# Kernel optimization log

Measured on AMD Instinct MI355X. Metric: run time of the kernel, lower is better.

Reference implementation:

```python
import jax, jax.numpy as jnp
import numpy as np
import math

B, S, H = 2, 2048, 1024
NH, HD = 16, 64
EPS = 1e-12


def setup_inputs() -> dict:
    key = jax.random.key(0)
    ks = jax.random.split(key, 6)
    scale = 1.0 / math.sqrt(H)
    return {
        "hidden_states": jax.random.normal(ks[0], (B, S, H), jnp.float32),
        "Wq": jax.random.normal(ks[1], (H, H), jnp.float32) * scale,
        "bq": jnp.zeros((H,), jnp.float32),
        "Wk": jax.random.normal(ks[2], (H, H), jnp.float32) * scale,
        "bk": jnp.zeros((H,), jnp.float32),
        "Wv": jax.random.normal(ks[3], (H, H), jnp.float32) * scale,
        "bv": jnp.zeros((H,), jnp.float32),
        "Wo": jax.random.normal(ks[4], (H, H), jnp.float32) * scale,
        "bo": jnp.zeros((H,), jnp.float32),
        "gamma": jnp.ones((H,), jnp.float32),
        "beta": jnp.zeros((H,), jnp.float32),
    }


def _heads(x):
    # [B, S, H] -> [B, NH, S, HD]
    return x.reshape(B, S, NH, HD).transpose(0, 2, 1, 3)


def reference(hidden_states, Wq, bq, Wk, bk, Wv, bv, Wo, bo, gamma, beta):
    q = _heads(hidden_states @ Wq + bq)
    k = _heads(hidden_states @ Wk + bk)
    v = _heads(hidden_states @ Wv + bv)
    # scores: [B, NH, S, S]
    scores = jnp.einsum("bhqd,bhkd->bhqk", q, k) / math.sqrt(HD)
    probs = jax.nn.softmax(scores, axis=-1)
    ctx = jnp.einsum("bhqk,bhkd->bhqd", probs, v)
    ctx = ctx.transpose(0, 2, 1, 3).reshape(B, S, H)
    attn_out = ctx @ Wo + bo
    x = attn_out + hidden_states
    mu = jnp.mean(x, axis=-1, keepdims=True)
    var = jnp.var(x, axis=-1, keepdims=True)
    return (x - mu) / jnp.sqrt(var + EPS) * gamma + beta
```

## Files before the change

kernel.cpp:

```cpp
#include <hip/hip_runtime.h>
#include <hip/hip_bf16.h>

#define B_ 2
#define S_ 2048
#define H_ 1024
#define NH_ 16
#define HD_ 64
#define M_ (B_*S_)

typedef __attribute__((ext_vector_type(8))) short bf16x8;
typedef __attribute__((ext_vector_type(4))) short bf16x4;
typedef __attribute__((ext_vector_type(4))) float f32x4;
typedef __attribute__((ext_vector_type(4))) int   i32x4;

__device__ inline float waveReduceSum(float v) {
#pragma unroll
  for (int off = 32; off >= 1; off >>= 1) v += __shfl_xor(v, off);
  return v;
}

__device__ inline short f2bf(float f) {
  union { float f; unsigned u; } v; v.f = f;
  unsigned r = v.u + 0x7fffu + ((v.u >> 16) & 1u);
  return (short)(r >> 16);
}

__device__ inline unsigned cvt_pk_bf16(float lo, float hi) {
  unsigned w;
  asm("v_cvt_pk_bf16_f32 %0, %1, %2" : "=v"(w) : "v"(lo), "v"(hi));
  return w;
}

__device__ inline void async_load16(const void* g, void* l) {
  __builtin_amdgcn_global_load_lds(
      (const __attribute__((address_space(1))) void*)g,
      (__attribute__((address_space(3))) void*)l, 16, 0, 0);
}

__device__ inline int swz8(int r) { return (r & 3) | (((r >> 3) & 1) << 2); }

__global__ __launch_bounds__(256)
void cvt_bf16(const float* __restrict__ in, short* __restrict__ out) {
  const size_t i = (size_t)blockIdx.x * 256 + threadIdx.x;
  float4 v = ((const float4*)in)[i];
  bf16x4 o;
  o[0] = f2bf(v.x); o[1] = f2bf(v.y); o[2] = f2bf(v.z); o[3] = f2bf(v.w);
  ((bf16x4*)out)[i] = o;
}

__global__ __launch_bounds__(256)
void transpose_w4(const float* __restrict__ W0, const float* __restrict__ W1,
                  const float* __restrict__ W2, const float* __restrict__ W3,
                  short* __restrict__ Tqkv, short* __restrict__ To) {
  const float* W; short* T;
  switch (blockIdx.z) {
    case 0: W = W0; T = Tqkv; break;
    case 1: W = W1; T = Tqkv + (size_t)1024 * 1024; break;
    case 2: W = W2; T = Tqkv + (size_t)2048 * 1024; break;
    default: W = W3; T = To; break;
  }
  __shared__ float tile[32][36];
  const int tid = threadIdx.x;
  const int tx = tid & 7, ty = tid >> 3;
  const int k0 = blockIdx.y << 5, n0 = blockIdx.x << 5;
  float4 v = *(const float4*)&W[(size_t)(k0 + ty) * H_ + n0 + (tx << 2)];
  tile[ty][(tx << 2) + 0] = v.x;
  tile[ty][(tx << 2) + 1] = v.y;
  tile[ty][(tx << 2) + 2] = v.z;
  tile[ty][(tx << 2) + 3] = v.w;
  __syncthreads();
  bf16x4 o;
  o[0] = f2bf(tile[(tx << 2) + 0][ty]);
  o[1] = f2bf(tile[(tx << 2) + 1][ty]);
  o[2] = f2bf(tile[(tx << 2) + 2][ty]);
  o[3] = f2bf(tile[(tx << 2) + 3][ty]);
  *(bf16x4*)&T[(size_t)(n0 + ty) * H_ + k0 + (tx << 2)] = o;
}

__global__ __launch_bounds__(256)
void gemm_qkv(const short* __restrict__ A, const short* __restrict__ Bt,
              const float* __restrict__ bq, const float* __restrict__ bk,
              const float* __restrict__ bv, short* __restrict__ Qo,
              short* __restrict__ Ko, short* __restrict__ Vto) {
  __shared__ short A_lds[2][128][32];
  __shared__ short B_lds[2][128][32];
  const int tid = threadIdx.x;
  const int lane = tid & 63, wv = tid >> 6;
  const int l16 = lane & 15, lg = lane >> 4;
  const int wr = wv >> 1, wc = wv & 1;
  const int swzb = (blockIdx.x & 7) * 96 + (blockIdx.x >> 3);
  const int bx = swzb % 24, by = swzb / 24;
  const int m0 = by << 7, n0 = bx << 7;
  const int K = H_;

  const int srow = lane >> 2, soff = (lane & 3) << 3;

  f32x4 acc[4][4] = {};

#pragma unroll
  for (int i = 0; i < 2; ++i) {
    const int c = 2 * wv + i;
    async_load16(A + (size_t)(m0 + 16 * c + srow) * K + soff, &A_lds[0][16 * c][0]);
    async_load16(Bt + (size_t)(n0 + 16 * c + srow) * K + soff, &B_lds[0][16 * c][0]);
  }

  int cur = 0;
  for (int t = 0; t < K / 32; ++t) {
    __syncthreads();
    if (t + 1 < K / 32) {
      const int k0 = (t + 1) << 5;
#pragma unroll
      for (int i = 0; i < 2; ++i) {
        const int c = 2 * wv + i;
        async_load16(A + (size_t)(m0 + 16 * c + srow) * K + k0 + soff,
                     &A_lds[cur ^ 1][16 * c][0]);
        async_load16(Bt + (size_t)(n0 + 16 * c + srow) * K + k0 + soff,
                     &B_lds[cur ^ 1][16 * c][0]);
      }
    }
    bf16x8 af[4], bfr[4];
#pragma unroll
    for (int i = 0; i < 4; ++i)
      af[i] = *(const bf16x8*)&A_lds[cur][64 * wr + 16 * i + l16][8 * lg];
#pragma unroll
    for (int j = 0; j < 4; ++j)
      bfr[j] = *(const bf16x8*)&B_lds[cur][64 * wc + 16 * j + l16][8 * lg];
#pragma unroll
    for (int i = 0; i < 4; ++i)
#pragma unroll
      for (int j = 0; j < 4; ++j)
        acc[i][j] = __builtin_amdgcn_mfma_f32_16x16x32_bf16(af[i], bfr[j], acc[i][j], 0, 0, 0);
    cur ^= 1;
  }

  const int mt = n0 >> 10;
  const float* bias = (mt == 0) ? bq : (mt == 1 ? bk : bv);
  const float qs = (mt == 0) ? 0.125f * 1.4426950408889634f : 1.0f;

  if (mt < 2) {
    short* Out = (mt == 0) ? Qo : Ko;
#pragma unroll
    for (int i = 0; i < 4; ++i) {
#pragma unroll
      for (int j = 0; j < 4; ++j) {
        const int nl = (n0 & 1023) + 64 * wc + 16 * j + l16;
        const float bvl = bias[nl];
        const int h = nl >> 6, d = nl & 63;
#pragma unroll
        for (int r = 0; r < 4; ++r) {
          const int m = m0 + 64 * wr + 16 * i + 4 * lg + r;
          const int b = m >> 11, s = m & (S_ - 1);
          Out[(((size_t)(b * NH_ + h) * S_ + s) << 6) + d] =
              f2bf((acc[i][j][r] + bvl) * qs);
        }
      }
    }
  } else {
#pragma unroll
    for (int i = 0; i < 4; ++i) {
      const int mb = m0 + 64 * wr + 16 * i + 4 * lg;
      const int b = mb >> 11, s = mb & (S_ - 1);
#pragma unroll
      for (int j = 0; j < 4; ++j) {
        const int nl = (n0 & 1023) + 64 * wc + 16 * j + l16;
        const float bvl = bias[nl];
        const int h = nl >> 6, d = nl & 63;
        bf16x4 pk;
#pragma unroll
        for (int r = 0; r < 4; ++r) pk[r] = f2bf(acc[i][j][r] + bvl);
        *(bf16x4*)&Vto[(((size_t)(b * NH_ + h) * HD_ + d) << 11) + s] = pk;
      }
    }
  }
}

__global__ __launch_bounds__(256)
void gemm_o(const short* __restrict__ A, const short* __restrict__ Bt,
            const float* __restrict__ bias, float* __restrict__ C) {
  __shared__ short A_lds[2][64][32];
  __shared__ short B_lds[2][128][32];
  const int tid = threadIdx.x;
  const int lane = tid & 63, wv = tid >> 6;
  const int l16 = lane & 15, lg = lane >> 4;
  const int wr = wv >> 1, wc = wv & 1;
  const int swzb = (blockIdx.x & 7) * 64 + (blockIdx.x >> 3);
  const int bx = swzb & 7, by = swzb >> 3;
  const int m0 = by << 6, n0 = bx << 7;
  const int K = H_;

  const int srow = lane >> 2, soff = (lane & 3) << 3;

  f32x4 acc[2][4] = {};

  async_load16(A + (size_t)(m0 + 16 * wv + srow) * K + soff, &A_lds[0][16 * wv][0]);
#pragma unroll
  for (int i = 0; i < 2; ++i) {
    const int c = 2 * wv + i;
    async_load16(Bt + (size_t)(n0 + 16 * c + srow) * K + soff, &B_lds[0][16 * c][0]);
  }

  int cur = 0;
  for (int t = 0; t < K / 32; ++t) {
    __syncthreads();
    if (t + 1 < K / 32) {
      const int k0 = (t + 1) << 5;
      async_load16(A + (size_t)(m0 + 16 * wv + srow) * K + k0 + soff,
                   &A_lds[cur ^ 1][16 * wv][0]);
#pragma unroll
      for (int i = 0; i < 2; ++i) {
        const int c = 2 * wv + i;
        async_load16(Bt + (size_t)(n0 + 16 * c + srow) * K + k0 + soff,
                     &B_lds[cur ^ 1][16 * c][0]);
      }
    }
    bf16x8 af[2], bfr[4];
#pragma unroll
    for (int i = 0; i < 2; ++i)
      af[i] = *(const bf16x8*)&A_lds[cur][32 * wr + 16 * i + l16][8 * lg];
#pragma unroll
    for (int j = 0; j < 4; ++j)
      bfr[j] = *(const bf16x8*)&B_lds[cur][64 * wc + 16 * j + l16][8 * lg];
#pragma unroll
    for (int i = 0; i < 2; ++i)
#pragma unroll
      for (int j = 0; j < 4; ++j)
        acc[i][j] = __builtin_amdgcn_mfma_f32_16x16x32_bf16(af[i], bfr[j], acc[i][j], 0, 0, 0);
    cur ^= 1;
  }

#pragma unroll
  for (int i = 0; i < 2; ++i)
#pragma unroll
    for (int j = 0; j < 4; ++j) {
      const int n = n0 + 64 * wc + 16 * j + l16;
      const float bvl = bias[n];
#pragma unroll
      for (int r = 0; r < 4; ++r) {
        const int m = m0 + 32 * wr + 16 * i + 4 * lg + r;
        C[(size_t)m * H_ + n] = acc[i][j][r] + bvl;
      }
    }
}

__global__ __launch_bounds__(256)
void attn_mfma(const short* __restrict__ Qg, const short* __restrict__ Kg,
               const short* __restrict__ Vtg, short* __restrict__ ctxb) {
  __shared__ short K_lds[2][2][64][64];
  __shared__ short V_t[2][2][64][64];

  const int tid  = threadIdx.x;
  const int lane = tid & 63;
  const int wv   = tid >> 6;
  const int l16  = lane & 15, lg = lane >> 4;

  const int swz = (blockIdx.x & 7) * 128 + (blockIdx.x >> 3);
  const int bh = swz >> 5, qb = swz & 31;

  const short* Qh = Qg + ((size_t)bh * S_ << 6);
  const short* Kh = Kg + ((size_t)bh * S_ << 6);
  const short* Vh = Vtg + ((size_t)bh << 6) * S_;

  const int q0 = qb * 64 + wv * 16;

  bf16x8 qf[2];
  qf[0] = *(const bf16x8*)&Qh[((size_t)(q0 + l16) << 6) + 8 * lg];
  qf[1] = *(const bf16x8*)&Qh[((size_t)(q0 + l16) << 6) + 8 * lg + 32];

  const int l16part = ((l16 >> 2) << 3) + (l16 & 3);

  const int kr = tid >> 2;
  const int cb = (tid & 3) << 1;
  const int sz = swz8(kr);
  const int c1 = ((cb    ) ^ sz) << 3;
  const int c2 = ((cb + 1) ^ sz) << 3;

  f32x4 o[4] = {};
  float m_run = -1e30f, l_run = 0.f;

#pragma unroll
  for (int h = 0; h < 2; ++h) {
    const size_t kg = ((size_t)(64 * h + kr)) << 6;
    *(bf16x8*)&K_lds[0][h][kr][c1] = *(const bf16x8*)&Kh[kg + (cb << 3)];
    *(bf16x8*)&K_lds[0][h][kr][c2] = *(const bf16x8*)&Kh[kg + ((cb + 1) << 3)];
    const size_t vg = (size_t)kr * S_ + 64 * h;
    *(bf16x8*)&V_t[0][h][kr][c1]   = *(const bf16x8*)&Vh[vg + (cb << 3)];
    *(bf16x8*)&V_t[0][h][kr][c2]   = *(const bf16x8*)&Vh[vg + ((cb + 1) << 3)];
  }

  int cur = 0;
  for (int t = 0; t < S_ / 128; ++t) {
    bf16x8 nk[2][2], nv[2][2];
    const bool pre = (t + 1 < S_ / 128);
    if (pre) {
      const int kvn = (t + 1) * 128;
#pragma unroll
      for (int h = 0; h < 2; ++h) {
        const size_t kb = ((size_t)(kvn + 64 * h + kr)) << 6;
        nk[h][0] = *(const bf16x8*)&Kh[kb + (cb << 3)];
        nk[h][1] = *(const bf16x8*)&Kh[kb + ((cb + 1) << 3)];
        const size_t vb = (size_t)kr * S_ + kvn + 64 * h;
        nv[h][0] = *(const bf16x8*)&Vh[vb + (cb << 3)];
        nv[h][1] = *(const bf16x8*)&Vh[vb + ((cb + 1) << 3)];
      }
    }
    __syncthreads();

    f32x4 s[2][4] = {};
    __builtin_amdgcn_s_setprio(1);
#pragma unroll
    for (int h = 0; h < 2; ++h)
#pragma unroll
      for (int ks = 0; ks < 2; ++ks)
#pragma unroll
        for (int tt = 0; tt < 4; ++tt) {
          const int krow = ((tt >> 1) << 5) + ((tt & 1) << 2) + l16part;
          const int kch = (lg + 4 * ks) ^ swz8(krow);
          bf16x8 kf = *(const bf16x8*)&K_lds[cur][h][krow][kch << 3];
          s[h][tt] = __builtin_amdgcn_mfma_f32_16x16x32_bf16(kf, qf[ks], s[h][tt], 0, 0, 0);
        }
    __builtin_amdgcn_s_setprio(0);

    float pmax = -1e30f;
#pragma unroll
    for (int h = 0; h < 2; ++h)
#pragma unroll
      for (int tt = 0; tt < 4; ++tt)
        pmax = fmaxf(pmax, fmaxf(fmaxf(s[h][tt][0], s[h][tt][1]),
                                 fmaxf(s[h][tt][2], s[h][tt][3])));
    pmax = fmaxf(pmax, __shfl_xor(pmax, 16));
    pmax = fmaxf(pmax, __shfl_xor(pmax, 32));

    float p[2][4][4];
    float rs = 0.f;
    if (__any(pmax - m_run > 8.0f)) {
      const float mn = fmaxf(m_run, pmax);
      const float scl = __builtin_amdgcn_exp2f(m_run - mn);
      m_run = mn;
#pragma unroll
      for (int h = 0; h < 2; ++h)
#pragma unroll
        for (int tt = 0; tt < 4; ++tt)
#pragma unroll
          for (int r = 0; r < 4; ++r) {
            p[h][tt][r] = __builtin_amdgcn_exp2f(s[h][tt][r] - mn);
            rs += p[h][tt][r];
          }
      rs += __shfl_xor(rs, 16);
      rs += __shfl_xor(rs, 32);
      l_run = l_run * scl + rs;
      float sclr[4];
#pragma unroll
      for (int r = 0; r < 4; ++r) sclr[r] = __shfl(scl, 4 * lg + r);
#pragma unroll
      for (int tt = 0; tt < 4; ++tt)
#pragma unroll
        for (int r = 0; r < 4; ++r) o[tt][r] *= sclr[r];
    } else {
#pragma unroll
      for (int h = 0; h < 2; ++h)
#pragma unroll
        for (int tt = 0; tt < 4; ++tt)
#pragma unroll
          for (int r = 0; r < 4; ++r) {
            p[h][tt][r] = __builtin_amdgcn_exp2f(s[h][tt][r] - m_run);
            rs += p[h][tt][r];
          }
      rs += __shfl_xor(rs, 16);
      rs += __shfl_xor(rs, 32);
      l_run += rs;
    }

    unsigned w[2][4][2];
#pragma unroll
    for (int h = 0; h < 2; ++h)
#pragma unroll
      for (int tt = 0; tt < 4; ++tt) {
        w[h][tt][0] = cvt_pk_bf16(p[h][tt][0], p[h][tt][1]);
        w[h][tt][1] = cvt_pk_bf16(p[h][tt][2], p[h][tt][3]);
      }

    __builtin_amdgcn_s_setprio(1);
#pragma unroll
    for (int h = 0; h < 2; ++h)
#pragma unroll
      for (int ks = 0; ks < 2; ++ks) {
        i32x4 aw;
        aw[0] = (int)w[h][2 * ks][0];
        aw[1] = (int)w[h][2 * ks][1];
        aw[2] = (int)w[h][2 * ks + 1][0];
        aw[3] = (int)w[h][2 * ks + 1][1];
        const bf16x8 pf = __builtin_bit_cast(bf16x8, aw);
#pragma unroll
        for (int tt = 0; tt < 4; ++tt) {
          const int vrow = 16 * tt + l16;
          const int vch = (lg + 4 * ks) ^ swz8(vrow);
          bf16x8 vf = *(const bf16x8*)&V_t[cur][h][vrow][vch << 3];
          o[tt] = __builtin_amdgcn_mfma_f32_16x16x32_bf16(pf, vf, o[tt], 0, 0, 0);
        }
      }
    __builtin_amdgcn_s_setprio(0);

    if (pre) {
#pragma unroll
      for (int h = 0; h < 2; ++h) {
        *(bf16x8*)&K_lds[cur ^ 1][h][kr][c1] = nk[h][0];
        *(bf16x8*)&K_lds[cur ^ 1][h][kr][c2] = nk[h][1];
        *(bf16x8*)&V_t[cur ^ 1][h][kr][c1]   = nv[h][0];
        *(bf16x8*)&V_t[cur ^ 1][h][kr][c2]   = nv[h][1];
      }
    }
    cur ^= 1;
  }

  float invr[4];
#pragma unroll
  for (int r = 0; r < 4; ++r) invr[r] = 1.f / __shfl(l_run, 4 * lg + r);
  const int b = bh >> 4, h = bh & 15;
#pragma unroll
  for (int r = 0; r < 4; ++r) {
    const int q = q0 + 4 * lg + r;
#pragma unroll
    for (int tt = 0; tt < 4; ++tt)
      ctxb[(((size_t)(b * S_ + q) * NH_ + h) << 6) + 16 * tt + l16] =
          f2bf(o[tt][r] * invr[r]);
  }
}

__global__ __launch_bounds__(256)
void resid_ln(const float* __restrict__ attn_out, const float* __restrict__ hs,
              const float* __restrict__ gamma, const float* __restrict__ beta,
              float* __restrict__ out) {
  __shared__ float reds[4], reds2[4];
  const int row = blockIdx.x;
  const int tid = threadIdx.x;
  const float4* a4 = (const float4*)(attn_out + ((size_t)row << 10));
  const float4* h4 = (const float4*)(hs + ((size_t)row << 10));
  float4 a = a4[tid], h = h4[tid];
  float e0 = a.x + h.x, e1 = a.y + h.y, e2 = a.z + h.z, e3 = a.w + h.w;
  float s  = e0 + e1 + e2 + e3;
  float sq = e0 * e0 + e1 * e1 + e2 * e2 + e3 * e3;
  s = waveReduceSum(s);
  sq = waveReduceSum(sq);
  const int lane = tid & 63, wave = tid >> 6;
  if (lane == 0) { reds[wave] = s; reds2[wave] = sq; }
  __syncthreads();
  const float S1 = reds[0] + reds[1] + reds[2] + reds[3];
  const float S2 = reds2[0] + reds2[1] + reds2[2] + reds2[3];
  const float mu = S1 * (1.f / H_);
  const float var = S2 * (1.f / H_) - mu * mu;
  const float rstd = rsqrtf(var + 1e-12f);
  const float4 g = ((const float4*)gamma)[tid];
  const float4 bb = ((const float4*)beta)[tid];
  float4 o;
  o.x = (e0 - mu) * rstd * g.x + bb.x;
  o.y = (e1 - mu) * rstd * g.y + bb.y;
  o.z = (e2 - mu) * rstd * g.z + bb.z;
  o.w = (e3 - mu) * rstd * g.w + bb.w;
  ((float4*)(out + ((size_t)row << 10)))[tid] = o;
}

extern "C" void kernel_launch(void* const* d_in, const int* in_sizes, int n_in,
                              void* d_out, int out_size, void* d_ws, size_t ws_size,
                              hipStream_t stream) {
  const float* X     = (const float*)d_in[0];
  const float* Wq    = (const float*)d_in[1];
  const float* bq    = (const float*)d_in[2];
  const float* Wk    = (const float*)d_in[3];
  const float* bk    = (const float*)d_in[4];
  const float* Wv    = (const float*)d_in[5];
  const float* bv    = (const float*)d_in[6];
  const float* Wo    = (const float*)d_in[7];
  const float* bo    = (const float*)d_in[8];
  const float* gamma = (const float*)d_in[9];
  const float* beta  = (const float*)d_in[10];
  float* out = (float*)d_out;

  char* ws = (char*)d_ws;
  short* Xbf  = (short*)ws;
  short* Wqkv = (short*)(ws + ( 8u << 20));
  short* Wto  = (short*)(ws + (14u << 20));
  short* Qbf  = (short*)(ws + (16u << 20));
  short* Kbf  = (short*)(ws + (24u << 20));
  short* Vt   = (short*)(ws + (32u << 20));
  short* ctxb = Xbf;
  float* attn = (float*)(ws + (16u << 20));

  dim3 blk(256);
  hipLaunchKernelGGL(cvt_bf16, dim3((M_ * H_) / 1024), blk, 0, stream, X, Xbf);
  hipLaunchKernelGGL(transpose_w4, dim3(32, 32, 4), blk, 0, stream,
                     Wq, Wk, Wv, Wo, Wqkv, Wto);
  hipLaunchKernelGGL(gemm_qkv, dim3(768), blk, 0, stream,
                     Xbf, Wqkv, bq, bk, bv, Qbf, Kbf, Vt);
  hipLaunchKernelGGL(attn_mfma, dim3(1024), blk, 0, stream, Qbf, Kbf, Vt, ctxb);
  hipLaunchKernelGGL(gemm_o, dim3(512), blk, 0, stream, ctxb, Wto, bo, attn);
  hipLaunchKernelGGL(resid_ln, dim3(M_), blk, 0, stream, attn, X, gamma, beta, out);
}
```

Baseline: 244.4 us.

## Enlarge QKV GEMM tile to 256x256 with 512 threads and explicit pipelining

The QKV projection GEMM moves from 128x128 tiles with 256 threads to 256x256 tiles with 512 threads (8 waves, 128x64 each), cutting the grid from 768 to 192 blocks. The load loop becomes a two-stage prefetch with explicit vmcnt waits, raw s_barrier calls, sched_barrier fences and setprio around the MFMA block. The goal is more operand reuse per LDS load and better overlap of global loads with MFMA work. In exchange, 192 blocks may leave part of the 256 CUs idle, and the 8x4 accumulator per wave raises register pressure.

```diff
diff --git a/kernel.cpp b/kernel.cpp
--- a/kernel.cpp
+++ b/kernel.cpp
@@ -77,61 +77,77 @@
   *(bf16x4*)&T[(size_t)(n0 + ty) * H_ + k0 + (tx << 2)] = o;
 }
 
-__global__ __launch_bounds__(256)
+#define QKV_NT 32
+
+__global__ __launch_bounds__(512)
 void gemm_qkv(const short* __restrict__ A, const short* __restrict__ Bt,
               const float* __restrict__ bq, const float* __restrict__ bk,
               const float* __restrict__ bv, short* __restrict__ Qo,
               short* __restrict__ Ko, short* __restrict__ Vto) {
-  __shared__ short A_lds[2][128][32];
-  __shared__ short B_lds[2][128][32];
+  __shared__ short A_lds[2][256][32];
+  __shared__ short B_lds[2][256][32];
   const int tid = threadIdx.x;
   const int lane = tid & 63, wv = tid >> 6;
   const int l16 = lane & 15, lg = lane >> 4;
-  const int wr = wv >> 1, wc = wv & 1;
-  const int swzb = (blockIdx.x & 7) * 96 + (blockIdx.x >> 3);
-  const int bx = swzb % 24, by = swzb / 24;
-  const int m0 = by << 7, n0 = bx << 7;
+  const int wr = wv >> 2, wc = wv & 3;
+  const int swzb = (blockIdx.x & 7) * 24 + (blockIdx.x >> 3);
+  const int bx = swzb % 12, by = swzb / 12;
+  const int m0 = by << 8, n0 = bx << 8;
   const int K = H_;
 
-  const int srow = lane >> 2, soff = (lane & 3) << 3;
-
-  f32x4 acc[4][4] = {};
-
-#pragma unroll
-  for (int i = 0; i < 2; ++i) {
-    const int c = 2 * wv + i;
-    async_load16(A + (size_t)(m0 + 16 * c + srow) * K + soff, &A_lds[0][16 * c][0]);
-    async_load16(Bt + (size_t)(n0 + 16 * c + srow) * K + soff, &B_lds[0][16 * c][0]);
-  }
-
-  int cur = 0;
-  for (int t = 0; t < K / 32; ++t) {
-    __syncthreads();
-    if (t + 1 < K / 32) {
-      const int k0 = (t + 1) << 5;
-#pragma unroll
-      for (int i = 0; i < 2; ++i) {
-        const int c = 2 * wv + i;
-        async_load16(A + (size_t)(m0 + 16 * c + srow) * K + k0 + soff,
-                     &A_lds[cur ^ 1][16 * c][0]);
-        async_load16(Bt + (size_t)(n0 + 16 * c + srow) * K + k0 + soff,
-                     &B_lds[cur ^ 1][16 * c][0]);
-      }
-    }
-    bf16x8 af[4], bfr[4];
-#pragma unroll
-    for (int i = 0; i < 4; ++i)
-      af[i] = *(const bf16x8*)&A_lds[cur][64 * wr + 16 * i + l16][8 * lg];
+  const int srow = lane >> 2;
+  const int sch  = lane & 3;
+
+#define QKV_STAGE(buf, t_)                                                     \
+  {                                                                            \
+    const int k0_ = (t_) << 5;                                                 \
+    _Pragma("unroll")                                                          \
+    for (int i_ = 0; i_ < 2; ++i_) {                                           \
+      const int r0_ = 128 * i_ + 16 * wv;                                      \
+      async_load16(A + (size_t)(m0 + r0_ + srow) * K + k0_ + (sch << 3),       \
+                   &A_lds[buf][r0_][0]);                                       \
+      async_load16(Bt + (size_t)(n0 + r0_ + srow) * K + k0_ + (sch << 3),      \
+                   &B_lds[buf][r0_][0]);                                       \
+    }                                                                          \
+  }
+
+  f32x4 acc[8][4] = {};
+
+  QKV_STAGE(0, 0)
+  QKV_STAGE(1, 1)
+  asm volatile("s_waitcnt vmcnt(4)" ::: "memory");
+  __builtin_amdgcn_s_barrier();
+  __builtin_amdgcn_sched_barrier(0);
+
+  for (int t = 0; t < QKV_NT; ++t) {
+    const int cur = t & 1;
+    bf16x8 af[8], bfr[4];
+#pragma unroll
+    for (int i = 0; i < 8; ++i)
+      af[i] = *(const bf16x8*)&A_lds[cur][128 * wr + 16 * i + l16][8 * lg];
 #pragma unroll
     for (int j = 0; j < 4; ++j)
       bfr[j] = *(const bf16x8*)&B_lds[cur][64 * wc + 16 * j + l16][8 * lg];
-#pragma unroll
-    for (int i = 0; i < 4; ++i)
+    __builtin_amdgcn_s_setprio(1);
+#pragma unroll
+    for (int i = 0; i < 8; ++i)
 #pragma unroll
       for (int j = 0; j < 4; ++j)
         acc[i][j] = __builtin_amdgcn_mfma_f32_16x16x32_bf16(af[i], bfr[j], acc[i][j], 0, 0, 0);
-    cur ^= 1;
-  }
+    __builtin_amdgcn_s_setprio(0);
+    __builtin_amdgcn_sched_barrier(0);
+    __builtin_amdgcn_s_barrier();
+    __builtin_amdgcn_sched_barrier(0);
+    if (t + 2 < QKV_NT) {
+      QKV_STAGE(cur, t + 2)
+      asm volatile("s_waitcnt vmcnt(4)" ::: "memory");
+    } else {
+      asm volatile("s_waitcnt vmcnt(0)" ::: "memory");
+    }
+    __builtin_amdgcn_s_barrier();
+    __builtin_amdgcn_sched_barrier(0);
+  }
+#undef QKV_STAGE
 
   const int mt = n0 >> 10;
   const float* bias = (mt == 0) ? bq : (mt == 1 ? bk : bv);
@@ -140,7 +156,7 @@
   if (mt < 2) {
     short* Out = (mt == 0) ? Qo : Ko;
 #pragma unroll
-    for (int i = 0; i < 4; ++i) {
+    for (int i = 0; i < 8; ++i) {
 #pragma unroll
       for (int j = 0; j < 4; ++j) {
         const int nl = (n0 & 1023) + 64 * wc + 16 * j + l16;
@@ -148,7 +164,7 @@
         const int h = nl >> 6, d = nl & 63;
 #pragma unroll
         for (int r = 0; r < 4; ++r) {
-          const int m = m0 + 64 * wr + 16 * i + 4 * lg + r;
+          const int m = m0 + 128 * wr + 16 * i + 4 * lg + r;
           const int b = m >> 11, s = m & (S_ - 1);
           Out[(((size_t)(b * NH_ + h) * S_ + s) << 6) + d] =
               f2bf((acc[i][j][r] + bvl) * qs);
@@ -157,8 +173,8 @@
     }
   } else {
 #pragma unroll
-    for (int i = 0; i < 4; ++i) {
-      const int mb = m0 + 64 * wr + 16 * i + 4 * lg;
+    for (int i = 0; i < 8; ++i) {
+      const int mb = m0 + 128 * wr + 16 * i + 4 * lg;
       const int b = mb >> 11, s = mb & (S_ - 1);
 #pragma unroll
       for (int j = 0; j < 4; ++j) {
@@ -489,7 +505,7 @@
   hipLaunchKernelGGL(cvt_bf16, dim3((M_ * H_) / 1024), blk, 0, stream, X, Xbf);
   hipLaunchKernelGGL(transpose_w4, dim3(32, 32, 4), blk, 0, stream,
                      Wq, Wk, Wv, Wo, Wqkv, Wto);
-  hipLaunchKernelGGL(gemm_qkv, dim3(768), blk, 0, stream,
+  hipLaunchKernelGGL(gemm_qkv, dim3(192), dim3(512), 0, stream,
                      Xbf, Wqkv, bq, bk, bv, Qbf, Kbf, Vt);
   hipLaunchKernelGGL(attn_mfma, dim3(1024), blk, 0, stream, Qbf, Kbf, Vt, ctxb);
   hipLaunchKernelGGL(gemm_o, dim3(512), blk, 0, stream, ctxb, Wto, bo, attn);
```

New measurement: 237.7 us. 2.8% less time.
